# Kernel optimization log

Measured on AMD Instinct MI355X. Metric: run time of the kernel, lower is better.

## Reference

```python
import jax, jax.numpy as jnp
import numpy as np

# Topology constants for size='large'
S = 490          # total switches: 128+64+64+96+64+32+32+10
W = 64           # n_wavelengths
M = 32           # n_modes
PS = 4           # patch_size
NPATCH = 49      # 7x7 patches of a 28x28 image
V1_START = 0
OUT_START = 480  # OUT region = last 10 switches
OUT_COUNT = 10
N_CLASSES = 10
SAT = 1.0        # cfg.saturation (not shown in source; standard value)
DECAY = 0.15
EPS = 1e-8


def encode_batch(images):
    """Real-valued patch encoding: [B,28,28] -> [B,49,64,32]."""
    B = images.shape[0]
    # unfold into non-overlapping 4x4 patches
    p = images[:, :7 * PS, :7 * PS].reshape(B, 7, PS, 7, PS)
    p = p.transpose(0, 1, 3, 2, 4).reshape(B, NPATCH, PS * PS)
    p = jnp.pad(p, ((0, 0), (0, 0), (0, M - PS * PS)))  # pad 16 -> 32 modes
    w_idx = jnp.arange(W, dtype=jnp.float32)
    w_weights = 1.0 - jnp.abs(w_idx - 32.0) / 64.0      # [W]
    return p[:, :, None, :] * w_weights[None, None, :, None]  # [B,NP,W,M]


def setup_inputs() -> dict:
    key = jax.random.key(0)
    k = jax.random.split(key, 7)
    images = jax.random.uniform(k[0], (8, 28, 28), dtype=jnp.float32)
    connectivity = jax.random.normal(k[1], (S, S), dtype=jnp.float32) * 0.05
    wavelength_weights = jax.random.uniform(k[2], (S, W), dtype=jnp.float32)
    switch_gain = jax.random.normal(k[3], (S,), dtype=jnp.float32) * 0.1
    switch_bias = jax.random.normal(k[4], (S,), dtype=jnp.float32) * 0.1
    readout_w = jax.random.normal(k[5], (N_CLASSES, OUT_COUNT), dtype=jnp.float32) * 0.1
    readout_b = jnp.zeros((N_CLASSES,), dtype=jnp.float32)
    return {
        "images": images,
        "connectivity": connectivity,
        "wavelength_weights": wavelength_weights,
        "switch_gain": switch_gain,
        "switch_bias": switch_bias,
        "readout_w": readout_w,
        "readout_b": readout_b,
        "n_steps": 15,
        "injection_steps": 5,
    }


def reference(images, connectivity, wavelength_weights, switch_gain, switch_bias,
              readout_w, readout_b, n_steps, injection_steps):
    B = images.shape[0]
    enc = encode_batch(images)                          # [B,49,W,M]
    enc_max = jnp.max(jnp.abs(enc))
    enc = jnp.where(enc_max > EPS, enc / enc_max, enc)
    inj = enc * 0.3                                     # injected signal (real; imag part is 0)

    gain = jax.nn.softplus(switch_gain)[None, :, None, None]
    bias = switch_bias[None, :, None, None]
    ww = wavelength_weights[None, :, :, None]

    field = jnp.zeros((B, S, W, M), jnp.float32)
    output = jnp.zeros((B, S, W, M), jnp.float32)

    def step(carry, t):
        field, output = carry
        # injection into V1 (min(v1_count=128, 49 patches) = 49) for t < injection_steps
        gate = jnp.where(t < injection_steps, 1.0, 0.0).astype(jnp.float32)
        field = field.at[:, V1_START:V1_START + NPATCH].add(gate * inj)
        # network step (complex magnitudes; imag is identically 0)
        out_mag = jnp.sqrt(output * output + EPS)
        gathered = jax.nn.relu(jnp.einsum('bswm,st->btwm', out_mag, connectivity))
        field_mag = jnp.sqrt(field * field + EPS) * (1.0 - DECAY) + gathered * 0.25
        weighted = field_mag * ww
        activated = SAT * jnp.tanh((weighted * gain + bias) / SAT)
        return (field_mag, activated), None

    (field, output), _ = jax.lax.scan(step, (field, output), jnp.arange(n_steps))

    out_field = output[:, OUT_START:OUT_START + OUT_COUNT]       # [B,10,W,M]
    out_energy = (out_field * out_field + EPS).sum(axis=(2, 3))  # [B,10]
    out_features = jnp.log1p(out_energy + EPS)
    return out_features @ readout_w.T + readout_b
```

## Files before the change

### kernel.cpp

```cpp
#include <hip/hip_runtime.h>
#include <math.h>

#define S_DIM 490
#define NPATCH 49
#define EPSF 1e-8f
#define SP 512
#define CI 8192
#define CPB 32
#define NBLK 256
#define HEAVY0 252
#define OMS 520

typedef __attribute__((ext_vector_type(8))) short bf16x8;
typedef __attribute__((ext_vector_type(4))) float f32x4;

__device__ __forceinline__ unsigned short f2bf(float x) {
    unsigned int u = __float_as_uint(x);
    unsigned int r = (u + 0x7FFF + ((u >> 16) & 1)) >> 16;
    return (unsigned short)r;
}
__device__ __forceinline__ float bf2f(unsigned short u) {
    return __uint_as_float(((unsigned int)u) << 16);
}

__global__ void k_max(const float* __restrict__ img, float* __restrict__ encmax) {
    __shared__ float red[256];
    float m = 0.f;
    for (int i = threadIdx.x; i < 8 * 28 * 28; i += 256)
        m = fmaxf(m, fabsf(img[i]));
    red[threadIdx.x] = m;
    __syncthreads();
    for (int s = 128; s > 0; s >>= 1) {
        if (threadIdx.x < s) red[threadIdx.x] = fmaxf(red[threadIdx.x], red[threadIdx.x + s]);
        __syncthreads();
    }
    if (threadIdx.x == 0) *encmax = red[0];
}

__global__ void k_prep(const float* __restrict__ ww, const float* __restrict__ sg,
                       const float* __restrict__ sb, float* __restrict__ K1,
                       float* __restrict__ K2) {
    int i = blockIdx.x * 256 + threadIdx.x;
    if (i < 64 * SP) {
        int w = i >> 9, t = i & (SP - 1);
        K1[i] = (t < S_DIM) ? ww[t * 64 + w] * log1pf(expf(sg[t])) : 0.f;
    }
    if (i < SP) K2[i] = (i < S_DIM) ? sb[i] : 0.f;
}

__global__ void k_g0(const float* __restrict__ conn, float* __restrict__ g0) {
    int t = blockIdx.x;
    float s = 0.f;
    if (t < S_DIM)
        for (int ss = threadIdx.x; ss < S_DIM; ss += 256)
            s += conn[ss * S_DIM + t];
    __shared__ float red[256];
    red[threadIdx.x] = s;
    __syncthreads();
    for (int st = 128; st > 0; st >>= 1) {
        if (threadIdx.x < st) red[threadIdx.x] += red[threadIdx.x + st];
        __syncthreads();
    }
    if (threadIdx.x == 0) g0[t] = (t < S_DIM) ? 0.25f * fmaxf(1e-4f * red[0], 0.f) : 0.f;
}

__global__ void k_connP(const float* __restrict__ conn, unsigned short* __restrict__ connP) {
    int i = blockIdx.x * 256 + threadIdx.x;
    int j    = i & 7;
    int lane = (i >> 3) & 63;
    int k    = (i >> 9) & 15;
    int tt   = (i >> 13) & 1;
    int strip = i >> 14;
    int t = strip * 32 + tt * 16 + (lane & 15);
    int s = k * 32 + (lane >> 4) * 8 + j;
    float v = (t < S_DIM && s < S_DIM) ? conn[s * S_DIM + t] : 0.f;
    connP[i] = f2bf(v);
}

__global__ void k_inj(const float* __restrict__ img, const float* __restrict__ encmax,
                      float* __restrict__ injT) {
    int i = blockIdx.x * 256 + threadIdx.x;
    int c = i >> 6, tt = i & 63;
    int b = c >> 10, w = (c >> 4) & 63, m = c & 15;
    float em = *encmax;
    float scale = (em > EPSF) ? (0.3f / em) : 0.3f;
    float v = 0.f;
    if (tt < NPATCH) {
        int r = (tt / 7) * 4 + (m >> 2);
        int col = (tt % 7) * 4 + (m & 3);
        float wgt = 1.0f - fabsf((float)w - 32.0f) * (1.0f / 64.0f);
        v = img[(b * 28 + r) * 28 + col] * wgt * scale;
    }
    injT[i] = v;
}

#define MFMA(A, B, C) __builtin_amdgcn_mfma_f32_16x16x32_bf16(A, B, C, 0, 0, 0)

__global__ __launch_bounds__(1024, 4) void k_run(
    const unsigned short* __restrict__ connP, const float* __restrict__ injT,
    const float* __restrict__ K1, const float* __restrict__ K2,
    const float* __restrict__ g0, const int* __restrict__ injSteps,
    float* __restrict__ partials, float* __restrict__ partialsS)
{
    __shared__ unsigned short om[2][48 * OMS];
    const int bk   = blockIdx.x;
    const int tid  = threadIdx.x;
    const int wv   = tid >> 6;
    const int lane = tid & 63;
    const int l16  = lane & 15, lq = lane >> 4;
    const bool heavy = (bk >= HEAVY0);
    const int c0 = bk * CPB;

    const int nInj = injSteps[0];
    const unsigned short* aP = connP + (size_t)(wv * 32) * 512 + lane * 8;

    f32x4 k1r[2][2], k2r[2], k1h[2];
    #pragma unroll
    for (int tt = 0; tt < 2; ++tt) {
        int t0 = (wv << 5) + tt * 16 + lq * 4;
        k2r[tt] = *(const f32x4*)(K2 + t0);
        #pragma unroll
        for (int cc = 0; cc < 2; ++cc) {
            int w = (2 * bk + cc) & 63;
            k1r[tt][cc] = *(const f32x4*)(K1 + w * SP + t0);
        }
        if (heavy) {
            int wsh = (bk - HEAVY0) * 16 + l16;
            k1h[tt] = *(const f32x4*)(K1 + wsh * SP + t0);
        }
    }

    const int rb0 = l16 * OMS;
    const int rb1 = (16 + l16) * OMS;
    const int rb2 = (32 + l16) * OMS;

    f32x4 fld[2][2] = {};
    f32x4 fld2[2] = {};

    {
        const bool inj0 = (wv < 2) && (0 < nInj);
        #pragma unroll
        for (int tt = 0; tt < 2; ++tt) {
            int t0 = (wv << 5) + tt * 16 + lq * 4;
            f32x4 g0v = *(const f32x4*)(g0 + t0);
            f32x4 k2 = k2r[tt];
            #pragma unroll
            for (int cc = 0; cc < 2; ++cc) {
                int cg = c0 + cc * 16 + l16;
                f32x4 k1 = k1r[tt][cc];
                f32x4 f = {};
                if (inj0) f = *(const f32x4*)(injT + (size_t)cg * 64 + t0);
                float o_[4];
                #pragma unroll
                for (int r = 0; r < 4; ++r) {
                    float fm = fabsf(f[r]) * 0.85f + g0v[r];
                    float x  = fabsf(fm * k1[r] + k2[r]);
                    float e  = exp2f(x * 2.8853900817779268f);
                    o_[r] = 1.f - 2.f * __builtin_amdgcn_rcpf(e + 1.f);
                    f[r] = fm;
                }
                fld[tt][cc] = f;
                unsigned int r01, r23;
                asm("v_cvt_pk_bf16_f32 %0, %1, %2" : "=v"(r01) : "v"(o_[0]), "v"(o_[1]));
                asm("v_cvt_pk_bf16_f32 %0, %1, %2" : "=v"(r23) : "v"(o_[2]), "v"(o_[3]));
                int cl = cc * 16 + l16;
                *(uint2*)&om[1][cl * OMS + t0] = make_uint2(r01, r23);
            }
            if (heavy) {
                f32x4 k1 = k1h[tt];
                float oh[4];
                f32x4 fh;
                #pragma unroll
                for (int r = 0; r < 4; ++r) {
                    float fm = g0v[r];
                    float x  = fabsf(fm * k1[r] + k2[r]);
                    float e  = exp2f(x * 2.8853900817779268f);
                    oh[r] = 1.f - 2.f * __builtin_amdgcn_rcpf(e + 1.f);
                    fh[r] = fm;
                }
                fld2[tt] = fh;
                unsigned int h01, h23;
                asm("v_cvt_pk_bf16_f32 %0, %1, %2" : "=v"(h01) : "v"(oh[0]), "v"(oh[1]));
                asm("v_cvt_pk_bf16_f32 %0, %1, %2" : "=v"(h23) : "v"(oh[2]), "v"(oh[3]));
                *(uint2*)&om[1][(32 + l16) * OMS + t0] = make_uint2(h01, h23);
            }
        }
    }
    __syncthreads();

    for (int st = 1; st < 15; ++st) {
        const unsigned short* bufR = om[st & 1];
        unsigned short* bufW = om[(st + 1) & 1];
        f32x4 acc[2][2] = {};
        f32x4 acc2[2] = {};
        __builtin_amdgcn_s_setprio(1);
        #pragma unroll 4
        for (int k = 0; k < 16; ++k) {
            bf16x8 a0 = *(const bf16x8*)(aP + (size_t)(k)      * 512);
            bf16x8 a1 = *(const bf16x8*)(aP + (size_t)(16 + k) * 512);
            int sOff = k * 32 + lq * 8;
            bf16x8 b0 = *(const bf16x8*)&bufR[rb0 + sOff];
            bf16x8 b1 = *(const bf16x8*)&bufR[rb1 + sOff];
            acc[0][0] = MFMA(a0, b0, acc[0][0]);
            acc[0][1] = MFMA(a0, b1, acc[0][1]);
            acc[1][0] = MFMA(a1, b0, acc[1][0]);
            acc[1][1] = MFMA(a1, b1, acc[1][1]);
            if (heavy) {
                bf16x8 b2 = *(const bf16x8*)&bufR[rb2 + sOff];
                acc2[0] = MFMA(a0, b2, acc2[0]);
                acc2[1] = MFMA(a1, b2, acc2[1]);
            }
        }
        __builtin_amdgcn_s_setprio(0);

        const bool injNow = (wv < 2) && (st < nInj);
        #pragma unroll
        for (int tt = 0; tt < 2; ++tt) {
            int t0 = (wv << 5) + tt * 16 + lq * 4;
            f32x4 k2 = k2r[tt];
            #pragma unroll
            for (int cc = 0; cc < 2; ++cc) {
                int cg = c0 + cc * 16 + l16;
                f32x4 k1 = k1r[tt][cc];
                f32x4 f = fld[tt][cc];
                if (injNow) f += *(const f32x4*)(injT + (size_t)cg * 64 + t0);
                f32x4 ac = acc[tt][cc];
                float o_[4];
                #pragma unroll
                for (int r = 0; r < 4; ++r) {
                    float g  = fmaxf(ac[r], 0.f);
                    float fm = fabsf(f[r]) * 0.85f + 0.25f * g;
                    float x  = fabsf(fm * k1[r] + k2[r]);
                    float e  = exp2f(x * 2.8853900817779268f);
                    o_[r] = 1.f - 2.f * __builtin_amdgcn_rcpf(e + 1.f);
                    f[r] = fm;
                }
                fld[tt][cc] = f;
                unsigned int r01, r23;
                asm("v_cvt_pk_bf16_f32 %0, %1, %2" : "=v"(r01) : "v"(o_[0]), "v"(o_[1]));
                asm("v_cvt_pk_bf16_f32 %0, %1, %2" : "=v"(r23) : "v"(o_[2]), "v"(o_[3]));
                int cl = cc * 16 + l16;
                *(uint2*)&bufW[cl * OMS + t0] = make_uint2(r01, r23);
            }
            if (heavy) {
                f32x4 k1 = k1h[tt];
                f32x4 fh = fld2[tt];
                f32x4 ah = acc2[tt];
                float oh[4];
                #pragma unroll
                for (int r = 0; r < 4; ++r) {
                    float g  = fmaxf(ah[r], 0.f);
                    float fm = fabsf(fh[r]) * 0.85f + 0.25f * g;
                    float x  = fabsf(fm * k1[r] + k2[r]);
                    float e  = exp2f(x * 2.8853900817779268f);
                    oh[r] = 1.f - 2.f * __builtin_amdgcn_rcpf(e + 1.f);
                    fh[r] = fm;
                }
                fld2[tt] = fh;
                unsigned int h01, h23;
                asm("v_cvt_pk_bf16_f32 %0, %1, %2" : "=v"(h01) : "v"(oh[0]), "v"(oh[1]));
                asm("v_cvt_pk_bf16_f32 %0, %1, %2" : "=v"(h23) : "v"(oh[2]), "v"(oh[3]));
                *(uint2*)&bufW[(32 + l16) * OMS + t0] = make_uint2(h01, h23);
            }
        }
        __syncthreads();
    }

    if (wv == 0) {
        int cl = (lane < 48) ? lane : 0;
        #pragma unroll
        for (int o = 0; o < 10; ++o) {
            float v = bf2f(om[1][cl * OMS + 480 + o]);
            float e = v * v;
            float em = (lane < 32) ? e : 0.f;
            em += __shfl_xor(em, 1);  em += __shfl_xor(em, 2);
            em += __shfl_xor(em, 4);  em += __shfl_xor(em, 8);
            em += __shfl_xor(em, 16);
            if (lane == 0) partials[bk * 10 + o] = em;
            if (heavy) {
                float es = (lane >= 32 && lane < 48) ? e : 0.f;
                es += __shfl_xor(es, 1); es += __shfl_xor(es, 2);
                es += __shfl_xor(es, 4); es += __shfl_xor(es, 8);
                if (lane == 32) partialsS[(bk - HEAVY0) * 10 + o] = es;
            }
        }
    }
}

__global__ void k_fin(const float* __restrict__ partials, const float* __restrict__ partialsS,
                      const float* __restrict__ rw, const float* __restrict__ rb,
                      float* __restrict__ out) {
    __shared__ float fe[80];
    int tid = threadIdx.x;
    if (tid < 80) {
        int b = tid / 10, o = tid % 10;
        float e = 0.f;
        #pragma unroll 8
        for (int j = 0; j < 32; ++j) e += partials[(b * 32 + j) * 10 + o];
        float es = 0.f;
        #pragma unroll
        for (int j = 0; j < 4; ++j) es += partialsS[j * 10 + o];
        e += 16.f * es + 2048.f * EPSF;
        fe[tid] = log1pf(e + EPSF);
    }
    __syncthreads();
    if (tid < 80) {
        int b = tid / 10, cls = tid % 10;
        float a = rb[cls];
        #pragma unroll
        for (int k = 0; k < 10; ++k) a += fe[b * 10 + k] * rw[cls * 10 + k];
        out[tid] = a;
    }
}

extern "C" void kernel_launch(void* const* d_in, const int* in_sizes, int n_in,
                              void* d_out, int out_size, void* d_ws, size_t ws_size,
                              hipStream_t stream) {
    (void)in_sizes; (void)n_in; (void)out_size; (void)ws_size;
    const float* img   = (const float*)d_in[0];
    const float* conn  = (const float*)d_in[1];
    const float* ww    = (const float*)d_in[2];
    const float* sgain = (const float*)d_in[3];
    const float* sbias = (const float*)d_in[4];
    const float* rw    = (const float*)d_in[5];
    const float* rb    = (const float*)d_in[6];
    const int* injsteps = (const int*)d_in[8];

    char* w = (char*)d_ws;
    unsigned short* connP = (unsigned short*)w;
    float* injT = (float*)(w + (size_t)SP * SP * 2);
    float* K1   = injT + (size_t)CI * 64;
    float* K2   = K1 + 64 * SP;
    float* g0   = K2 + SP;
    float* encmax    = g0 + SP;
    float* partials  = encmax + 4;
    float* partialsS = partials + NBLK * 10;

    k_max  <<<1, 256, 0, stream>>>(img, encmax);
    k_prep <<<128, 256, 0, stream>>>(ww, sgain, sbias, K1, K2);
    k_g0   <<<SP, 256, 0, stream>>>(conn, g0);
    k_connP<<<(SP * SP) / 256, 256, 0, stream>>>(conn, connP);
    k_inj  <<<(CI * 64) / 256, 256, 0, stream>>>(img, encmax, injT);

    k_run<<<NBLK, 1024, 0, stream>>>(connP, injT, K1, K2, g0, injsteps, partials, partialsS);
    k_fin<<<1, 128, 0, stream>>>(partials, partialsS, rw, rb, (float*)d_out);
}
```

Measured before the change: 127.8 us.

## Stream connectivity through per-wave LDS ring via global_load_lds and swizzle state buffer

Result: slower. 266.3 us (+108.4%).

```diff
diff --git a/kernel.cpp b/kernel.cpp
--- a/kernel.cpp
+++ b/kernel.cpp
@@ -9,7 +9,8 @@
 #define CPB 32
 #define NBLK 256
 #define HEAVY0 252
-#define OMS 520
+#define OMHALF (48 * 512)
+#define RINGOFF (2 * OMHALF)
 
 typedef __attribute__((ext_vector_type(8))) short bf16x8;
 typedef __attribute__((ext_vector_type(4))) float f32x4;
@@ -21,6 +22,11 @@
 }
 __device__ __forceinline__ float bf2f(unsigned short u) {
     return __uint_as_float(((unsigned int)u) << 16);
+}
+__device__ __forceinline__ void gload16(const void* g, void* l) {
+    __builtin_amdgcn_global_load_lds(
+        (const __attribute__((address_space(1))) unsigned int*)g,
+        (__attribute__((address_space(3))) unsigned int*)l, 16, 0, 0);
 }
 
 __global__ void k_max(const float* __restrict__ img, float* __restrict__ encmax) {
@@ -102,7 +108,7 @@
     const float* __restrict__ g0, const int* __restrict__ injSteps,
     float* __restrict__ partials, float* __restrict__ partialsS)
 {
-    __shared__ unsigned short om[2][48 * OMS];
+    __shared__ unsigned short LDSA[RINGOFF + 16 * 2 * 2 * 512];
     const int bk   = blockIdx.x;
     const int tid  = threadIdx.x;
     const int wv   = tid >> 6;
@@ -112,7 +118,13 @@
     const int c0 = bk * CPB;
 
     const int nInj = injSteps[0];
-    const unsigned short* aP = connP + (size_t)(wv * 32) * 512 + lane * 8;
+
+    unsigned short* rs00 = &LDSA[RINGOFF + ((wv * 2 + 0) * 2 + 0) * 512];
+    unsigned short* rs01 = &LDSA[RINGOFF + ((wv * 2 + 0) * 2 + 1) * 512];
+    unsigned short* rs10 = &LDSA[RINGOFF + ((wv * 2 + 1) * 2 + 0) * 512];
+    unsigned short* rs11 = &LDSA[RINGOFF + ((wv * 2 + 1) * 2 + 1) * 512];
+    const unsigned short* gA0 = connP + (size_t)(wv * 32) * 512 + lane * 8;
+    const unsigned short* gA1 = gA0 + 16 * 512;
 
     f32x4 k1r[2][2], k2r[2], k1h[2];
     #pragma unroll
@@ -130,12 +142,17 @@
         }
     }
 
-    const int rb0 = l16 * OMS;
-    const int rb1 = (16 + l16) * OMS;
-    const int rb2 = (32 + l16) * OMS;
+    const int msk = (l16 & 7) << 3;
+    const int lo  = (lq * 8) ^ (msk & 24);
+    const int s5  = msk & 32;
+    const int be0 = l16 * 512 + lo + s5;
+    const int bo0 = l16 * 512 + lo + (32 ^ s5);
+    const int be1 = be0 + 16 * 512, bo1 = bo0 + 16 * 512;
+    const int be2 = be0 + 32 * 512, bo2 = bo0 + 32 * 512;
 
     f32x4 fld[2][2] = {};
     f32x4 fld2[2] = {};
+    unsigned short* om1 = LDSA + OMHALF;
 
     {
         const bool inj0 = (wv < 2) && (0 < nInj);
@@ -164,7 +181,7 @@
                 asm("v_cvt_pk_bf16_f32 %0, %1, %2" : "=v"(r01) : "v"(o_[0]), "v"(o_[1]));
                 asm("v_cvt_pk_bf16_f32 %0, %1, %2" : "=v"(r23) : "v"(o_[2]), "v"(o_[3]));
                 int cl = cc * 16 + l16;
-                *(uint2*)&om[1][cl * OMS + t0] = make_uint2(r01, r23);
+                *(uint2*)&om1[(cl * 512 + t0) ^ ((cl & 7) << 3)] = make_uint2(r01, r23);
             }
             if (heavy) {
                 f32x4 k1 = k1h[tt];
@@ -182,34 +199,56 @@
                 unsigned int h01, h23;
                 asm("v_cvt_pk_bf16_f32 %0, %1, %2" : "=v"(h01) : "v"(oh[0]), "v"(oh[1]));
                 asm("v_cvt_pk_bf16_f32 %0, %1, %2" : "=v"(h23) : "v"(oh[2]), "v"(oh[3]));
-                *(uint2*)&om[1][(32 + l16) * OMS + t0] = make_uint2(h01, h23);
-            }
-        }
-    }
+                int cl = 32 + l16;
+                *(uint2*)&om1[(cl * 512 + t0) ^ ((cl & 7) << 3)] = make_uint2(h01, h23);
+            }
+        }
+    }
+    gload16(gA0, rs00);
+    gload16(gA1, rs01);
+    gload16(gA0 + 512, rs10);
+    gload16(gA1 + 512, rs11);
     __syncthreads();
 
     for (int st = 1; st < 15; ++st) {
-        const unsigned short* bufR = om[st & 1];
-        unsigned short* bufW = om[(st + 1) & 1];
+        const unsigned short* bufR = LDSA + (st & 1) * OMHALF;
+        unsigned short* bufW = LDSA + ((st + 1) & 1) * OMHALF;
         f32x4 acc[2][2] = {};
         f32x4 acc2[2] = {};
+        bf16x8 b0c = *(const bf16x8*)&bufR[be0];
+        bf16x8 b1c = *(const bf16x8*)&bufR[be1];
         __builtin_amdgcn_s_setprio(1);
-        #pragma unroll 4
+        #pragma unroll
         for (int k = 0; k < 16; ++k) {
-            bf16x8 a0 = *(const bf16x8*)(aP + (size_t)(k)      * 512);
-            bf16x8 a1 = *(const bf16x8*)(aP + (size_t)(16 + k) * 512);
-            int sOff = k * 32 + lq * 8;
-            bf16x8 b0 = *(const bf16x8*)&bufR[rb0 + sOff];
-            bf16x8 b1 = *(const bf16x8*)&bufR[rb1 + sOff];
-            acc[0][0] = MFMA(a0, b0, acc[0][0]);
-            acc[0][1] = MFMA(a0, b1, acc[0][1]);
-            acc[1][0] = MFMA(a1, b0, acc[1][0]);
-            acc[1][1] = MFMA(a1, b1, acc[1][1]);
+            asm volatile("s_waitcnt vmcnt(2)" ::: "memory");
+            const unsigned short* r0 = (k & 1) ? rs10 : rs00;
+            const unsigned short* r1 = (k & 1) ? rs11 : rs01;
+            bf16x8 a0 = *(const bf16x8*)(r0 + lane * 8);
+            bf16x8 a1 = *(const bf16x8*)(r1 + lane * 8);
+            bf16x8 b0n = b0c, b1n = b1c;
+            if (k < 15) {
+                int off0 = ((k + 1) & 1) ? (bo0 + k * 32) : (be0 + (k + 1) * 32);
+                int off1 = ((k + 1) & 1) ? (bo1 + k * 32) : (be1 + (k + 1) * 32);
+                b0n = *(const bf16x8*)&bufR[off0];
+                b1n = *(const bf16x8*)&bufR[off1];
+            }
+            acc[0][0] = MFMA(a0, b0c, acc[0][0]);
+            acc[0][1] = MFMA(a0, b1c, acc[0][1]);
+            acc[1][0] = MFMA(a1, b0c, acc[1][0]);
+            acc[1][1] = MFMA(a1, b1c, acc[1][1]);
             if (heavy) {
-                bf16x8 b2 = *(const bf16x8*)&bufR[rb2 + sOff];
+                int offh = (k & 1) ? (bo2 + (k - 1) * 32) : (be2 + k * 32);
+                bf16x8 b2 = *(const bf16x8*)&bufR[offh];
                 acc2[0] = MFMA(a0, b2, acc2[0]);
                 acc2[1] = MFMA(a1, b2, acc2[1]);
             }
+            __builtin_amdgcn_sched_barrier(0);
+            {
+                int kn = (k + 2) & 15;
+                gload16(gA0 + (size_t)kn * 512, (k & 1) ? rs10 : rs00);
+                gload16(gA1 + (size_t)kn * 512, (k & 1) ? rs11 : rs01);
+            }
+            b0c = b0n; b1c = b1n;
         }
         __builtin_amdgcn_s_setprio(0);
 
@@ -240,7 +279,7 @@
                 asm("v_cvt_pk_bf16_f32 %0, %1, %2" : "=v"(r01) : "v"(o_[0]), "v"(o_[1]));
                 asm("v_cvt_pk_bf16_f32 %0, %1, %2" : "=v"(r23) : "v"(o_[2]), "v"(o_[3]));
                 int cl = cc * 16 + l16;
-                *(uint2*)&bufW[cl * OMS + t0] = make_uint2(r01, r23);
+                *(uint2*)&bufW[(cl * 512 + t0) ^ ((cl & 7) << 3)] = make_uint2(r01, r23);
             }
             if (heavy) {
                 f32x4 k1 = k1h[tt];
@@ -260,7 +299,8 @@
                 unsigned int h01, h23;
                 asm("v_cvt_pk_bf16_f32 %0, %1, %2" : "=v"(h01) : "v"(oh[0]), "v"(oh[1]));
                 asm("v_cvt_pk_bf16_f32 %0, %1, %2" : "=v"(h23) : "v"(oh[2]), "v"(oh[3]));
-                *(uint2*)&bufW[(32 + l16) * OMS + t0] = make_uint2(h01, h23);
+                int cl = 32 + l16;
+                *(uint2*)&bufW[(cl * 512 + t0) ^ ((cl & 7) << 3)] = make_uint2(h01, h23);
             }
         }
         __syncthreads();
@@ -270,7 +310,7 @@
         int cl = (lane < 48) ? lane : 0;
         #pragma unroll
         for (int o = 0; o < 10; ++o) {
-            float v = bf2f(om[1][cl * OMS + 480 + o]);
+            float v = bf2f(om1[(cl * 512 + 480 + o) ^ ((cl & 7) << 3)]);
             float e = v * v;
             float em = (lane < 32) ? e : 0.f;
             em += __shfl_xor(em, 1);  em += __shfl_xor(em, 2);
```
